# Kernel tuning notes

Measured on AMD Instinct MI355X. Metric: run time of the kernel, lower is better.

The kernel has to match this reference:

```python
import jax, jax.numpy as jnp
import numpy as np

B, QUE, VAL, D = 4, 128, 128, 512

def setup_inputs() -> dict:
    key = jax.random.key(0)
    k = jax.random.split(key, 8)
    return {
        "qs_1": jax.random.normal(k[0], (B, QUE, D), jnp.float32),
        "qs_2": jax.random.normal(k[1], (B, QUE, D), jnp.float32),  # unused by forward, kept for signature fidelity
        "ks":   jax.random.normal(k[2], (B, VAL, D), jnp.float32),
        "vs":   jax.random.normal(k[3], (B, VAL, D), jnp.float32),
        "sg_mask": jax.random.randint(k[4], (B, VAL), 0, 2).astype(bool),  # True = masked
        "W1":  jax.random.normal(k[5], (D, D), jnp.float32) / np.sqrt(D),
        "b1":  jnp.zeros((D,), jnp.float32),
        "Wse": jax.random.normal(k[6], (D, D), jnp.float32) / np.sqrt(D),
        "bse": jnp.zeros((D,), jnp.float32),
        "W2":  jax.random.normal(k[7], (D, 1), jnp.float32) / np.sqrt(D),
        "b2":  jnp.zeros((1,), jnp.float32),
    }

def reference(qs_1, qs_2, ks, vs, sg_mask, W1, b1, Wse, bse, W2, b2):
    # Pairwise query-key elementwise product: [B, que, val, d]
    x = qs_1[:, :, None, :] * ks[:, None, :, :]
    # linear1: Linear(d,d) + ReLU (dropout = identity at eval)
    h = jax.nn.relu(jnp.einsum('bqvd,de->bqve', x, W1) + b1)
    # linear2: Linear(d,1) + ReLU -> scalar score per (q, v) pair
    s = jax.nn.relu(jnp.einsum('bqvd,do->bqvo', h, W2) + b2)[..., 0]  # [B, que, val]
    m = sg_mask[:, None, :]                      # [B, 1, val], True = masked out
    # masked mean of h over the val axis (masked_fill(0) then divide by valid count)
    h = jnp.where(m[..., None], 0.0, h)
    denom = jnp.sum(~sg_mask, axis=-1).astype(h.dtype)      # [B]
    mean = h.sum(axis=2) / denom[:, None, None]             # [B, que, d]
    # squeeze-excitation gate: sigmoid(relu(Linear(d,d)))
    gate = jax.nn.sigmoid(jax.nn.relu(mean @ Wse + bse))    # [B, que, d]
    # masked softmax over val, weighted sum of values
    s = jnp.where(m, -1e9, s)
    w = jax.nn.softmax(s, axis=-1)                          # [B, que, val]
    out = jnp.einsum('bqv,bvd->bqd', w, vs)                 # [B, que, d]
    return gate * out
```

## Files before the change

kernel.cpp:

```cpp
#include <hip/hip_runtime.h>
#include <stdint.h>
#include <stddef.h>

#define BDIM 4
#define QUE  128
#define VAL  128
#define DD   512
#define BQ   (BDIM*QUE)
#define BK   64

typedef float    f32x4 __attribute__((ext_vector_type(4)));
typedef float    f32x2 __attribute__((ext_vector_type(2)));
typedef _Float16 f16x8 __attribute__((ext_vector_type(8)));
typedef _Float16 f16x4 __attribute__((ext_vector_type(4)));
typedef _Float16 f16x2 __attribute__((ext_vector_type(2)));

typedef const __attribute__((address_space(1))) void* gas_ptr;
typedef __attribute__((address_space(3))) void*       las_ptr;

__device__ __forceinline__ void async_copy16(const void* g, void* l) {
    __builtin_amdgcn_global_load_lds((gas_ptr)g, (las_ptr)l, 16, 0, 0);
}

__global__ __launch_bounds__(256) void prep_kernel(const float* __restrict__ W1,
                                                   _Float16* __restrict__ W1T,
                                                   const float* __restrict__ Wse,
                                                   _Float16* __restrict__ WseT,
                                                   const float* __restrict__ vs,
                                                   _Float16* __restrict__ vsT,
                                                   const float* __restrict__ qs1,
                                                   _Float16* __restrict__ qH,
                                                   const float* __restrict__ ks,
                                                   _Float16* __restrict__ ksH) {
    const int gx = blockIdx.x, gy = blockIdx.y;
    if (gy >= 36) {
        const float* src = (gy == 36) ? qs1 : ks;
        _Float16*    dst = (gy == 36) ? qH  : ksH;
        size_t base = (size_t)gx * 16384 + threadIdx.x * 4;
        #pragma unroll 4
        for (int i = 0; i < 16; ++i) {
            f32x4 w = *(const f32x4*)(src + base + (size_t)i * 1024);
            f16x4 h;
            h[0] = (_Float16)w[0]; h[1] = (_Float16)w[1];
            h[2] = (_Float16)w[2]; h[3] = (_Float16)w[3];
            *(f16x4*)(dst + base + (size_t)i * 1024) = h;
        }
        return;
    }
    __shared__ float tile[32][33];
    const int tx = threadIdx.x & 31;
    const int ty = threadIdx.x >> 5;
    if (gy < 32) {
        const float* src = (gy < 16) ? W1  : Wse;
        _Float16*    dst = (gy < 16) ? W1T : WseT;
        int a0 = gx * 32;
        int b0 = (gy & 15) * 32;
        #pragma unroll
        for (int r = 0; r < 4; ++r)
            tile[ty + r*8][tx] = src[(size_t)(a0 + ty + r*8) * DD + b0 + tx];
        __syncthreads();
        #pragma unroll
        for (int r = 0; r < 4; ++r) {
            int el = ty + r*8;
            dst[(size_t)(b0 + el) * DD + a0 + tx] = (_Float16)tile[tx][el];
        }
    } else {
        int bb = gy - 32;
        const float* src = vs  + (size_t)bb * VAL * DD;
        _Float16*    dst = vsT + (size_t)bb * DD * VAL;
        int b0 = gx * 32;
        for (int vt = 0; vt < 4; ++vt) {
            int a0 = vt * 32;
            __syncthreads();
            #pragma unroll
            for (int r = 0; r < 4; ++r)
                tile[ty + r*8][tx] = src[(size_t)(a0 + ty + r*8) * DD + b0 + tx];
            __syncthreads();
            #pragma unroll
            for (int r = 0; r < 4; ++r) {
                int el = ty + r*8;
                dst[(size_t)(b0 + el) * VAL + a0 + tx] = (_Float16)tile[tx][el];
            }
        }
    }
}

__global__ __launch_bounds__(512, 4) void gemm_h_kernel(
    const _Float16* __restrict__ qH,
    const _Float16* __restrict__ ksH,
    const int*   __restrict__ sgmask,
    const _Float16* __restrict__ W1T,
    const float* __restrict__ b1,
    const float* __restrict__ W2,
    float* __restrict__ s_part,
    float* __restrict__ meansum)
{
    __shared__ _Float16 Ah[128 * BK];
    __shared__ _Float16 Bh[256 * BK];
    __shared__ float sred[4][VAL];
    __shared__ float msumLDS[2][256];

    const int tid  = threadIdx.x;
    const int bq   = blockIdx.x;
    const int gy   = blockIdx.y;
    const int b    = bq >> 7;
    const int lane = tid & 63;
    const int wid  = tid >> 6;
    const int wm   = wid >> 2;
    const int wn   = wid & 3;
    const int quad = lane >> 4;
    const int lr   = lane & 15;

    f32x4 acc[4][4];
    #pragma unroll
    for (int i = 0; i < 4; ++i)
        #pragma unroll
        for (int j = 0; j < 4; ++j) acc[i][j] = (f32x4){0.f, 0.f, 0.f, 0.f};

    const int ar0 = tid >> 3;
    const int slt = tid & 7;
    const int ca0 = (slt - (ar0 & 7)) & 7;
    const _Float16* ksrow0 = ksH + ((size_t)b * VAL + ar0)      * DD + ca0 * 8;
    const _Float16* ksrow1 = ksH + ((size_t)b * VAL + 64 + ar0) * DD + ca0 * 8;
    const _Float16* qrow_g = qH  + (size_t)bq * DD + ca0 * 8;
    const int aoff0 = tid * 8;
    const int aoff1 = (512 + tid) * 8;

    const _Float16* gB[4];
    int ldsBoff[4];
    #pragma unroll
    for (int j = 0; j < 4; ++j) {
        int chunk = j * 512 + tid;
        int row   = chunk >> 3;
        int c     = ((chunk & 7) - (row & 7)) & 7;
        gB[j] = W1T + (size_t)(gy * 256 + row) * DD + c * 8;
        ldsBoff[j] = (j * 512 + wid * 64) * 8;
    }

    int faoff[4], fboff[4];
    #pragma unroll
    for (int mt = 0; mt < 4; ++mt) {
        int row = wm * 64 + mt * 16 + lr;
        faoff[mt] = row * BK + (((quad + row) & 7) << 3);
    }
    #pragma unroll
    for (int nt = 0; nt < 4; ++nt) {
        int row = wn * 64 + nt * 16 + lr;
        fboff[nt] = row * BK + (((quad + row) & 7) << 3);
    }

    f16x8 kv0 = *(const f16x8*)(ksrow0);
    f16x8 kv1 = *(const f16x8*)(ksrow1);
    f16x8 qv  = *(const f16x8*)(qrow_g);

    for (int i = 0; i < 8; ++i) {
        const int kk = i * BK;
        #pragma unroll
        for (int j = 0; j < 4; ++j)
            async_copy16(gB[j] + kk, &Bh[ldsBoff[j]]);
        *(f16x8*)&Ah[aoff0] = kv0 * qv;
        *(f16x8*)&Ah[aoff1] = kv1 * qv;
        __syncthreads();

        if (i < 7) {
            kv0 = *(const f16x8*)(ksrow0 + kk + BK);
            kv1 = *(const f16x8*)(ksrow1 + kk + BK);
            qv  = *(const f16x8*)(qrow_g + kk + BK);
        }
        #pragma unroll
        for (int sub = 0; sub < 2; ++sub) {
            const int sx = sub << 5;
            f16x8 fa[4];
            #pragma unroll
            for (int mt = 0; mt < 4; ++mt)
                fa[mt] = *(const f16x8*)&Ah[faoff[mt] ^ sx];
            #pragma unroll
            for (int nt = 0; nt < 4; ++nt) {
                f16x8 fb = *(const f16x8*)&Bh[fboff[nt] ^ sx];
                #pragma unroll
                for (int mt = 0; mt < 4; ++mt)
                    acc[mt][nt] = __builtin_amdgcn_mfma_f32_16x16x32_f16(fa[mt], fb, acc[mt][nt], 0, 0, 0);
            }
        }
        __syncthreads();
    }

    float b1v[4], w2v[4];
    #pragma unroll
    for (int nt = 0; nt < 4; ++nt) {
        int col = gy*256 + wn*64 + nt*16 + lr;
        b1v[nt] = b1[col];
        w2v[nt] = W2[col];
    }
    float msum[4] = {0.f, 0.f, 0.f, 0.f};
    #pragma unroll
    for (int mt = 0; mt < 4; ++mt) {
        #pragma unroll
        for (int reg = 0; reg < 4; ++reg) {
            int v = wm*64 + mt*16 + quad*4 + reg;
            int masked = sgmask[b * VAL + v];
            float sacc = 0.f;
            #pragma unroll
            for (int nt = 0; nt < 4; ++nt) {
                float h = acc[mt][nt][reg] + b1v[nt];
                h = fmaxf(h, 0.f);
                sacc += h * w2v[nt];
                if (!masked) msum[nt] += h;
            }
            sacc += __shfl_xor(sacc, 1);
            sacc += __shfl_xor(sacc, 2);
            sacc += __shfl_xor(sacc, 4);
            sacc += __shfl_xor(sacc, 8);
            if (lr == 0) sred[wn][v] = sacc;
        }
    }
    #pragma unroll
    for (int nt = 0; nt < 4; ++nt) {
        float m = msum[nt];
        m += __shfl_xor(m, 16);
        m += __shfl_xor(m, 32);
        if (lane < 16) msumLDS[wm][wn*64 + nt*16 + lr] = m;
    }
    __syncthreads();
    if (tid < 128) {
        s_part[((size_t)bq * 2 + gy) * VAL + tid] =
            sred[0][tid] + sred[1][tid] + sred[2][tid] + sred[3][tid];
    } else if (tid >= 256) {
        int c = tid - 256;
        meansum[(size_t)bq * DD + gy*256 + c] = msumLDS[0][c] + msumLDS[1][c];
    }
}

#define MPAD 514
#define WPAD 130
__global__ __launch_bounds__(256) void final_kernel(
    const float* __restrict__ s_part,
    const float* __restrict__ msum,
    const int*   __restrict__ sgmask,
    const _Float16* __restrict__ WseT,
    const _Float16* __restrict__ vsT,
    const float* __restrict__ bse,
    const float* __restrict__ b2,
    float* __restrict__ out)
{
    __shared__ _Float16 meanLDS[32 * MPAD];
    __shared__ _Float16 wLDS[32 * WPAD];
    __shared__ _Float16 BLDS[32 * WPAD];

    const int tid  = threadIdx.x;
    const int q0   = blockIdx.x * 32;
    const int d0   = blockIdx.y * 32;
    const int b    = q0 >> 7;
    const int lane = tid & 63;
    const int wid  = tid >> 6;
    const int wm   = wid >> 1, wn = wid & 1;
    const int quad = lane >> 4;
    const int lr   = lane & 15;
    const int r    = tid >> 3;
    const int sl   = tid & 7;

    const float b2v = b2[0];
    const int   bq  = q0 + r;
    const float* sp = s_part + (size_t)bq * 2 * VAL;
    float vals[16];
    int   msk[16];
    float smax = -3.4e38f;
    #pragma unroll
    for (int i4 = 0; i4 < 4; ++i4) {
        f32x4 s0 = *(const f32x4*)(sp + sl*16 + i4*4);
        f32x4 s1 = *(const f32x4*)(sp + VAL + sl*16 + i4*4);
        #pragma unroll
        for (int j = 0; j < 4; ++j) {
            int idx = i4*4 + j;
            int v   = sl*16 + idx;
            float s = fmaxf(s0[j] + s1[j] + b2v, 0.f);
            int m   = sgmask[b * VAL + v];
            msk[idx] = m;
            if (m) s = -1e9f;
            vals[idx] = s;
            smax = fmaxf(smax, s);
        }
    }
    smax = fmaxf(smax, __shfl_xor(smax, 1));
    smax = fmaxf(smax, __shfl_xor(smax, 2));
    smax = fmaxf(smax, __shfl_xor(smax, 4));
    float sume = 0.f, cnt = 0.f;
    #pragma unroll
    for (int i = 0; i < 16; ++i) {
        vals[i] = __expf(vals[i] - smax);
        sume += vals[i];
        cnt  += msk[i] ? 0.f : 1.f;
    }
    sume += __shfl_xor(sume, 1);  cnt += __shfl_xor(cnt, 1);
    sume += __shfl_xor(sume, 2);  cnt += __shfl_xor(cnt, 2);
    sume += __shfl_xor(sume, 4);  cnt += __shfl_xor(cnt, 4);
    const float invse = 1.f / sume;
    const float invd  = 1.f / cnt;
    f16x8 wv0, wv1;
    #pragma unroll
    for (int i = 0; i < 8; ++i) {
        wv0[i] = (_Float16)(vals[i]     * invse);
        wv1[i] = (_Float16)(vals[i + 8] * invse);
    }
    *(f16x8*)&wLDS[r * WPAD + sl*16]     = wv0;
    *(f16x8*)&wLDS[r * WPAD + sl*16 + 8] = wv1;
    const float* mrow = msum + (size_t)bq * DD;
    #pragma unroll
    for (int i = 0; i < 8; ++i) {
        int e = i*64 + sl*8;
        f32x4 m0 = *(const f32x4*)(mrow + e);
        f32x4 m1 = *(const f32x4*)(mrow + e + 4);
        f16x8 mh;
        #pragma unroll
        for (int c = 0; c < 4; ++c) {
            mh[c]     = (_Float16)(m0[c] * invd);
            mh[c + 4] = (_Float16)(m1[c] * invd);
        }
        *(f16x8*)&meanLDS[r * MPAD + e] = mh;
    }
    __syncthreads();

    f32x4 accg = (f32x4){0.f, 0.f, 0.f, 0.f};
    const int a_off = (wm*16 + lr) * MPAD + quad*8;
    const int b_off = (wn*16 + lr) * WPAD + quad*8;
    const int st_off = r * WPAD + sl*16;
    #pragma unroll
    for (int cc = 0; cc < 4; ++cc) {
        const _Float16* wrow = WseT + (size_t)(d0 + r) * DD + cc*128 + sl*16;
        f16x8 bw0 = *(const f16x8*)(wrow);
        f16x8 bw1 = *(const f16x8*)(wrow + 8);
        *(f16x8*)&BLDS[st_off]     = bw0;
        *(f16x8*)&BLDS[st_off + 8] = bw1;
        __syncthreads();
        #pragma unroll
        for (int ks = 0; ks < 4; ++ks) {
            f16x8 fa = *(const f16x8*)&meanLDS[a_off + cc*128 + ks*32];
            f16x8 fb = *(const f16x8*)&BLDS[b_off + ks*32];
            accg = __builtin_amdgcn_mfma_f32_16x16x32_f16(fa, fb, accg, 0, 0, 0);
        }
        __syncthreads();
    }

    {
        const _Float16* vrow = vsT + ((size_t)b * DD + d0 + r) * VAL + sl*16;
        f16x8 bv0 = *(const f16x8*)(vrow);
        f16x8 bv1 = *(const f16x8*)(vrow + 8);
        *(f16x8*)&BLDS[st_off]     = bv0;
        *(f16x8*)&BLDS[st_off + 8] = bv1;
    }
    __syncthreads();
    f32x4 acco = (f32x4){0.f, 0.f, 0.f, 0.f};
    const int w_off = (wm*16 + lr) * WPAD + quad*8;
    #pragma unroll
    for (int ks = 0; ks < 4; ++ks) {
        f16x8 fa = *(const f16x8*)&wLDS[w_off + ks*32];
        f16x8 fb = *(const f16x8*)&BLDS[b_off + ks*32];
        acco = __builtin_amdgcn_mfma_f32_16x16x32_f16(fa, fb, acco, 0, 0, 0);
    }

    const int d = d0 + wn*16 + lr;
    const float bsev = bse[d];
    #pragma unroll
    for (int reg = 0; reg < 4; ++reg) {
        int q = q0 + wm*16 + quad*4 + reg;
        float g = fmaxf(accg[reg] + bsev, 0.f);
        g = 1.f / (1.f + __expf(-g));
        out[(size_t)q * DD + d] = g * acco[reg];
    }
}

extern "C" void kernel_launch(void* const* d_in, const int* in_sizes, int n_in,
                              void* d_out, int out_size, void* d_ws, size_t ws_size,
                              hipStream_t stream) {
    (void)in_sizes; (void)n_in; (void)out_size; (void)ws_size;
    const float* qs1 = (const float*)d_in[0];
    const float* ks  = (const float*)d_in[2];
    const float* vs  = (const float*)d_in[3];
    const int*   sg  = (const int*)d_in[4];
    const float* W1  = (const float*)d_in[5];
    const float* b1  = (const float*)d_in[6];
    const float* Wse = (const float*)d_in[7];
    const float* bse = (const float*)d_in[8];
    const float* W2  = (const float*)d_in[9];
    const float* b2  = (const float*)d_in[10];
    float* out = (float*)d_out;

    char* ws = (char*)d_ws;
    _Float16* W1T    = (_Float16*)(ws);
    _Float16* WseT   = (_Float16*)(ws + (512 << 10));
    _Float16* vsT    = (_Float16*)(ws + (1 << 20));
    float*    s_part = (float*)(ws + (1536 << 10));
    float*    msum   = (float*)(ws + (2 << 20));
    _Float16* qH     = (_Float16*)(ws + (3 << 20));
    _Float16* ksH    = (_Float16*)(ws + (3 << 20) + (512 << 10));

    prep_kernel<<<dim3(16, 38), 256, 0, stream>>>(W1, W1T, Wse, WseT, vs, vsT,
                                                  qs1, qH, ks, ksH);
    gemm_h_kernel<<<dim3(BQ, 2), 512, 0, stream>>>(qH, ksH, sg, W1T, b1, W2, s_part, msum);
    final_kernel<<<dim3(16, 16), 256, 0, stream>>>(s_part, msum, sg, WseT, vsT, bse, b2, out);
}
```

Measured before the change: 128.4 us.

## Split prep work across more blocks and preload final-kernel operands into LDS

```diff
diff --git a/kernel.cpp b/kernel.cpp
--- a/kernel.cpp
+++ b/kernel.cpp
@@ -10,10 +10,8 @@
 #define BK   64
 
 typedef float    f32x4 __attribute__((ext_vector_type(4)));
-typedef float    f32x2 __attribute__((ext_vector_type(2)));
 typedef _Float16 f16x8 __attribute__((ext_vector_type(8)));
 typedef _Float16 f16x4 __attribute__((ext_vector_type(4)));
-typedef _Float16 f16x2 __attribute__((ext_vector_type(2)));
 
 typedef const __attribute__((address_space(1))) void* gas_ptr;
 typedef __attribute__((address_space(3))) void*       las_ptr;
@@ -33,12 +31,12 @@
                                                    const float* __restrict__ ks,
                                                    _Float16* __restrict__ ksH) {
     const int gx = blockIdx.x, gy = blockIdx.y;
-    if (gy >= 36) {
-        const float* src = (gy == 36) ? qs1 : ks;
-        _Float16*    dst = (gy == 36) ? qH  : ksH;
-        size_t base = (size_t)gx * 16384 + threadIdx.x * 4;
-        #pragma unroll 4
-        for (int i = 0; i < 16; ++i) {
+    if (gy >= 48) {
+        const float* src = (gy < 50) ? qs1 : ks;
+        _Float16*    dst = (gy < 50) ? qH  : ksH;
+        size_t base = ((size_t)(gy & 1) * 16 + gx) * 8192 + threadIdx.x * 4;
+        #pragma unroll
+        for (int i = 0; i < 8; ++i) {
             f32x4 w = *(const f32x4*)(src + base + (size_t)i * 1024);
             f16x4 h;
             h[0] = (_Float16)w[0]; h[1] = (_Float16)w[1];
@@ -50,38 +48,33 @@
     __shared__ float tile[32][33];
     const int tx = threadIdx.x & 31;
     const int ty = threadIdx.x >> 5;
+    const float* src;
+    _Float16*    dst;
+    int a0, b0, dstride;
     if (gy < 32) {
-        const float* src = (gy < 16) ? W1  : Wse;
-        _Float16*    dst = (gy < 16) ? W1T : WseT;
-        int a0 = gx * 32;
-        int b0 = (gy & 15) * 32;
-        #pragma unroll
-        for (int r = 0; r < 4; ++r)
-            tile[ty + r*8][tx] = src[(size_t)(a0 + ty + r*8) * DD + b0 + tx];
-        __syncthreads();
-        #pragma unroll
-        for (int r = 0; r < 4; ++r) {
-            int el = ty + r*8;
-            dst[(size_t)(b0 + el) * DD + a0 + tx] = (_Float16)tile[tx][el];
-        }
+        src = (gy < 16) ? W1  : Wse;
+        dst = (gy < 16) ? W1T : WseT;
+        a0 = gx * 32;
+        b0 = (gy & 15) * 32;
+        dstride = DD;
     } else {
-        int bb = gy - 32;
-        const float* src = vs  + (size_t)bb * VAL * DD;
-        _Float16*    dst = vsT + (size_t)bb * DD * VAL;
-        int b0 = gx * 32;
-        for (int vt = 0; vt < 4; ++vt) {
-            int a0 = vt * 32;
-            __syncthreads();
-            #pragma unroll
-            for (int r = 0; r < 4; ++r)
-                tile[ty + r*8][tx] = src[(size_t)(a0 + ty + r*8) * DD + b0 + tx];
-            __syncthreads();
-            #pragma unroll
-            for (int r = 0; r < 4; ++r) {
-                int el = ty + r*8;
-                dst[(size_t)(b0 + el) * VAL + a0 + tx] = (_Float16)tile[tx][el];
-            }
-        }
+        const int j  = gy - 32;
+        const int bb = j >> 2;
+        const int vt = j & 3;
+        src = vs  + (size_t)bb * VAL * DD;
+        dst = vsT + (size_t)bb * DD * VAL;
+        a0 = vt * 32;
+        b0 = gx * 32;
+        dstride = VAL;
+    }
+    #pragma unroll
+    for (int r = 0; r < 4; ++r)
+        tile[ty + r*8][tx] = src[(size_t)(a0 + ty + r*8) * DD + b0 + tx];
+    __syncthreads();
+    #pragma unroll
+    for (int r = 0; r < 4; ++r) {
+        int el = ty + r*8;
+        dst[(size_t)(b0 + el) * dstride + a0 + tx] = (_Float16)tile[tx][el];
     }
 }
 
@@ -244,8 +237,9 @@
     float* __restrict__ out)
 {
     __shared__ _Float16 meanLDS[32 * MPAD];
+    __shared__ _Float16 BW[32 * MPAD];
     __shared__ _Float16 wLDS[32 * WPAD];
-    __shared__ _Float16 BLDS[32 * WPAD];
+    __shared__ _Float16 BV[32 * WPAD];
 
     const int tid  = threadIdx.x;
     const int q0   = blockIdx.x * 32;
@@ -259,6 +253,22 @@
     const int r    = tid >> 3;
     const int sl   = tid & 7;
 
+    {
+        const _Float16* wrow = WseT + (size_t)(d0 + r) * DD + sl*16;
+        #pragma unroll
+        for (int cc = 0; cc < 4; ++cc) {
+            f16x8 bw0 = *(const f16x8*)(wrow + cc*128);
+            f16x8 bw1 = *(const f16x8*)(wrow + cc*128 + 8);
+            *(f16x8*)&BW[r * MPAD + cc*128 + sl*16]     = bw0;
+            *(f16x8*)&BW[r * MPAD + cc*128 + sl*16 + 8] = bw1;
+        }
+        const _Float16* vrow = vsT + ((size_t)b * DD + d0 + r) * VAL + sl*16;
+        f16x8 bv0 = *(const f16x8*)(vrow);
+        f16x8 bv1 = *(const f16x8*)(vrow + 8);
+        *(f16x8*)&BV[r * WPAD + sl*16]     = bv0;
+        *(f16x8*)&BV[r * WPAD + sl*16 + 8] = bv1;
+    }
+
     const float b2v = b2[0];
     const int   bq  = q0 + r;
     const float* sp = s_part + (size_t)bq * 2 * VAL;
@@ -318,43 +328,33 @@
         }
         *(f16x8*)&meanLDS[r * MPAD + e] = mh;
     }
+
     __syncthreads();
 
-    f32x4 accg = (f32x4){0.f, 0.f, 0.f, 0.f};
+    f32x4 accg0 = (f32x4){0.f, 0.f, 0.f, 0.f};
+    f32x4 accg1 = (f32x4){0.f, 0.f, 0.f, 0.f};
     const int a_off = (wm*16 + lr) * MPAD + quad*8;
-    const int b_off = (wn*16 + lr) * WPAD + quad*8;
-    const int st_off = r * WPAD + sl*16;
+    const int bg_off = (wn*16 + lr) * MPAD + quad*8;
     #pragma unroll
     for (int cc = 0; cc < 4; ++cc) {
-        const _Float16* wrow = WseT + (size_t)(d0 + r) * DD + cc*128 + sl*16;
-        f16x8 bw0 = *(const f16x8*)(wrow);
-        f16x8 bw1 = *(const f16x8*)(wrow + 8);
-        *(f16x8*)&BLDS[st_off]     = bw0;
-        *(f16x8*)&BLDS[st_off + 8] = bw1;
-        __syncthreads();
         #pragma unroll
         for (int ks = 0; ks < 4; ++ks) {
             f16x8 fa = *(const f16x8*)&meanLDS[a_off + cc*128 + ks*32];
-            f16x8 fb = *(const f16x8*)&BLDS[b_off + ks*32];
-            accg = __builtin_amdgcn_mfma_f32_16x16x32_f16(fa, fb, accg, 0, 0, 0);
-        }
-        __syncthreads();
-    }
-
-    {
-        const _Float16* vrow = vsT + ((size_t)b * DD + d0 + r) * VAL + sl*16;
-        f16x8 bv0 = *(const f16x8*)(vrow);
-        f16x8 bv1 = *(const f16x8*)(vrow + 8);
-        *(f16x8*)&BLDS[st_off]     = bv0;
-        *(f16x8*)&BLDS[st_off + 8] = bv1;
-    }
-    __syncthreads();
+            f16x8 fb = *(const f16x8*)&BW[bg_off + cc*128 + ks*32];
+            if (((cc*4 + ks) & 1) == 0)
+                accg0 = __builtin_amdgcn_mfma_f32_16x16x32_f16(fa, fb, accg0, 0, 0, 0);
+            else
+                accg1 = __builtin_amdgcn_mfma_f32_16x16x32_f16(fa, fb, accg1, 0, 0, 0);
+        }
+    }
+
     f32x4 acco = (f32x4){0.f, 0.f, 0.f, 0.f};
     const int w_off = (wm*16 + lr) * WPAD + quad*8;
+    const int bv_off = (wn*16 + lr) * WPAD + quad*8;
     #pragma unroll
     for (int ks = 0; ks < 4; ++ks) {
         f16x8 fa = *(const f16x8*)&wLDS[w_off + ks*32];
-        f16x8 fb = *(const f16x8*)&BLDS[b_off + ks*32];
+        f16x8 fb = *(const f16x8*)&BV[bv_off + ks*32];
         acco = __builtin_amdgcn_mfma_f32_16x16x32_f16(fa, fb, acco, 0, 0, 0);
     }
 
@@ -363,7 +363,7 @@
     #pragma unroll
     for (int reg = 0; reg < 4; ++reg) {
         int q = q0 + wm*16 + quad*4 + reg;
-        float g = fmaxf(accg[reg] + bsev, 0.f);
+        float g = fmaxf(accg0[reg] + accg1[reg] + bsev, 0.f);
         g = 1.f / (1.f + __expf(-g));
         out[(size_t)q * DD + d] = g * acco[reg];
     }
@@ -394,7 +394,7 @@
     _Float16* qH     = (_Float16*)(ws + (3 << 20));
     _Float16* ksH    = (_Float16*)(ws + (3 << 20) + (512 << 10));
 
-    prep_kernel<<<dim3(16, 38), 256, 0, stream>>>(W1, W1T, Wse, WseT, vs, vsT,
+    prep_kernel<<<dim3(16, 52), 256, 0, stream>>>(W1, W1T, Wse, WseT, vs, vsT,
                                                   qs1, qH, ks, ksH);
     gemm_h_kernel<<<dim3(BQ, 2), 512, 0, stream>>>(qH, ksH, sg, W1T, b1, W2, s_part, msum);
     final_kernel<<<dim3(16, 16), 256, 0, stream>>>(s_part, msum, sg, WseT, vsT, bse, b2, out);
```

Result: no change. 126.0 us (-1.8%).

## Fuse final gating and softmax-weighted sum into the H GEMM kernel

Applied to the files above, without the earlier changes.

```diff
diff --git a/kernel.cpp b/kernel.cpp
--- a/kernel.cpp
+++ b/kernel.cpp
@@ -10,7 +10,6 @@
 #define BK   64
 
 typedef float    f32x4 __attribute__((ext_vector_type(4)));
-typedef float    f32x2 __attribute__((ext_vector_type(2)));
 typedef _Float16 f16x8 __attribute__((ext_vector_type(8)));
 typedef _Float16 f16x4 __attribute__((ext_vector_type(4)));
 typedef _Float16 f16x2 __attribute__((ext_vector_type(2)));
@@ -26,19 +25,18 @@
                                                    _Float16* __restrict__ W1T,
                                                    const float* __restrict__ Wse,
                                                    _Float16* __restrict__ WseT,
-                                                   const float* __restrict__ vs,
-                                                   _Float16* __restrict__ vsT,
                                                    const float* __restrict__ qs1,
                                                    _Float16* __restrict__ qH,
                                                    const float* __restrict__ ks,
                                                    _Float16* __restrict__ ksH) {
     const int gx = blockIdx.x, gy = blockIdx.y;
-    if (gy >= 36) {
-        const float* src = (gy == 36) ? qs1 : ks;
-        _Float16*    dst = (gy == 36) ? qH  : ksH;
-        size_t base = (size_t)gx * 16384 + threadIdx.x * 4;
-        #pragma unroll 4
-        for (int i = 0; i < 16; ++i) {
+    if (gy >= 32) {
+        const int jj = gy - 32;
+        const float* src = (jj < 2) ? qs1 : ks;
+        _Float16*    dst = (jj < 2) ? qH  : ksH;
+        size_t base = ((size_t)(jj & 1) * 16 + gx) * 8192 + threadIdx.x * 4;
+        #pragma unroll
+        for (int i = 0; i < 8; ++i) {
             f32x4 w = *(const f32x4*)(src + base + (size_t)i * 1024);
             f16x4 h;
             h[0] = (_Float16)w[0]; h[1] = (_Float16)w[1];
@@ -50,38 +48,18 @@
     __shared__ float tile[32][33];
     const int tx = threadIdx.x & 31;
     const int ty = threadIdx.x >> 5;
-    if (gy < 32) {
-        const float* src = (gy < 16) ? W1  : Wse;
-        _Float16*    dst = (gy < 16) ? W1T : WseT;
-        int a0 = gx * 32;
-        int b0 = (gy & 15) * 32;
-        #pragma unroll
-        for (int r = 0; r < 4; ++r)
-            tile[ty + r*8][tx] = src[(size_t)(a0 + ty + r*8) * DD + b0 + tx];
-        __syncthreads();
-        #pragma unroll
-        for (int r = 0; r < 4; ++r) {
-            int el = ty + r*8;
-            dst[(size_t)(b0 + el) * DD + a0 + tx] = (_Float16)tile[tx][el];
-        }
-    } else {
-        int bb = gy - 32;
-        const float* src = vs  + (size_t)bb * VAL * DD;
-        _Float16*    dst = vsT + (size_t)bb * DD * VAL;
-        int b0 = gx * 32;
-        for (int vt = 0; vt < 4; ++vt) {
-            int a0 = vt * 32;
-            __syncthreads();
-            #pragma unroll
-            for (int r = 0; r < 4; ++r)
-                tile[ty + r*8][tx] = src[(size_t)(a0 + ty + r*8) * DD + b0 + tx];
-            __syncthreads();
-            #pragma unroll
-            for (int r = 0; r < 4; ++r) {
-                int el = ty + r*8;
-                dst[(size_t)(b0 + el) * VAL + a0 + tx] = (_Float16)tile[tx][el];
-            }
-        }
+    const float* src = (gy < 16) ? W1  : Wse;
+    _Float16*    dst = (gy < 16) ? W1T : WseT;
+    const int a0 = gx * 32;
+    const int b0 = (gy & 15) * 32;
+    #pragma unroll
+    for (int r = 0; r < 4; ++r)
+        tile[ty + r*8][tx] = src[(size_t)(a0 + ty + r*8) * DD + b0 + tx];
+    __syncthreads();
+    #pragma unroll
+    for (int r = 0; r < 4; ++r) {
+        int el = ty + r*8;
+        dst[(size_t)(b0 + el) * DD + a0 + tx] = (_Float16)tile[tx][el];
     }
 }
 
@@ -92,17 +70,22 @@
     const _Float16* __restrict__ W1T,
     const float* __restrict__ b1,
     const float* __restrict__ W2,
-    float* __restrict__ s_part,
-    float* __restrict__ meansum)
+    const _Float16* __restrict__ WseT,
+    const float* __restrict__ bse,
+    const float* __restrict__ b2,
+    const float* __restrict__ vs,
+    float* __restrict__ out)
 {
     __shared__ _Float16 Ah[128 * BK];
     __shared__ _Float16 Bh[256 * BK];
-    __shared__ float sred[4][VAL];
-    __shared__ float msumLDS[2][256];
+    __shared__ float sredP[4][VAL];
+    __shared__ float msumP2[2][DD];
+    __shared__ float w_lds[VAL];
+    __shared__ _Float16 mean_h[DD];
+    __shared__ float scal[1];
 
     const int tid  = threadIdx.x;
     const int bq   = blockIdx.x;
-    const int gy   = blockIdx.y;
     const int b    = bq >> 7;
     const int lane = tid & 63;
     const int wid  = tid >> 6;
@@ -110,12 +93,6 @@
     const int wn   = wid & 3;
     const int quad = lane >> 4;
     const int lr   = lane & 15;
-
-    f32x4 acc[4][4];
-    #pragma unroll
-    for (int i = 0; i < 4; ++i)
-        #pragma unroll
-        for (int j = 0; j < 4; ++j) acc[i][j] = (f32x4){0.f, 0.f, 0.f, 0.f};
 
     const int ar0 = tid >> 3;
     const int slt = tid & 7;
@@ -133,7 +110,7 @@
         int chunk = j * 512 + tid;
         int row   = chunk >> 3;
         int c     = ((chunk & 7) - (row & 7)) & 7;
-        gB[j] = W1T + (size_t)(gy * 256 + row) * DD + c * 8;
+        gB[j] = W1T + (size_t)row * DD + c * 8;
         ldsBoff[j] = (j * 512 + wid * 64) * 8;
     }
 
@@ -149,224 +126,156 @@
         fboff[nt] = row * BK + (((quad + row) & 7) << 3);
     }
 
-    f16x8 kv0 = *(const f16x8*)(ksrow0);
-    f16x8 kv1 = *(const f16x8*)(ksrow1);
-    f16x8 qv  = *(const f16x8*)(qrow_g);
-
-    for (int i = 0; i < 8; ++i) {
-        const int kk = i * BK;
-        #pragma unroll
-        for (int j = 0; j < 4; ++j)
-            async_copy16(gB[j] + kk, &Bh[ldsBoff[j]]);
-        *(f16x8*)&Ah[aoff0] = kv0 * qv;
-        *(f16x8*)&Ah[aoff1] = kv1 * qv;
-        __syncthreads();
-
-        if (i < 7) {
-            kv0 = *(const f16x8*)(ksrow0 + kk + BK);
-            kv1 = *(const f16x8*)(ksrow1 + kk + BK);
-            qv  = *(const f16x8*)(qrow_g + kk + BK);
-        }
-        #pragma unroll
-        for (int sub = 0; sub < 2; ++sub) {
-            const int sx = sub << 5;
-            f16x8 fa[4];
-            #pragma unroll
-            for (int mt = 0; mt < 4; ++mt)
-                fa[mt] = *(const f16x8*)&Ah[faoff[mt] ^ sx];
-            #pragma unroll
-            for (int nt = 0; nt < 4; ++nt) {
-                f16x8 fb = *(const f16x8*)&Bh[fboff[nt] ^ sx];
+    for (int pass = 0; pass < 2; ++pass) {
+        const size_t poff = (size_t)pass * 256 * DD;
+
+        f32x4 acc[4][4];
+        #pragma unroll
+        for (int i = 0; i < 4; ++i)
+            #pragma unroll
+            for (int j = 0; j < 4; ++j) acc[i][j] = (f32x4){0.f, 0.f, 0.f, 0.f};
+
+        f16x8 kv0 = *(const f16x8*)(ksrow0);
+        f16x8 kv1 = *(const f16x8*)(ksrow1);
+        f16x8 qv  = *(const f16x8*)(qrow_g);
+
+        for (int i = 0; i < 8; ++i) {
+            const int kk = i * BK;
+            #pragma unroll
+            for (int j = 0; j < 4; ++j)
+                async_copy16(gB[j] + poff + kk, &Bh[ldsBoff[j]]);
+            *(f16x8*)&Ah[aoff0] = kv0 * qv;
+            *(f16x8*)&Ah[aoff1] = kv1 * qv;
+            __syncthreads();
+
+            if (i < 7) {
+                kv0 = *(const f16x8*)(ksrow0 + kk + BK);
+                kv1 = *(const f16x8*)(ksrow1 + kk + BK);
+                qv  = *(const f16x8*)(qrow_g + kk + BK);
+            }
+            #pragma unroll
+            for (int sub = 0; sub < 2; ++sub) {
+                const int sx = sub << 5;
+                f16x8 fa[4];
                 #pragma unroll
                 for (int mt = 0; mt < 4; ++mt)
-                    acc[mt][nt] = __builtin_amdgcn_mfma_f32_16x16x32_f16(fa[mt], fb, acc[mt][nt], 0, 0, 0);
+                    fa[mt] = *(const f16x8*)&Ah[faoff[mt] ^ sx];
+                #pragma unroll
+                for (int nt = 0; nt < 4; ++nt) {
+                    f16x8 fb = *(const f16x8*)&Bh[fboff[nt] ^ sx];
+                    #pragma unroll
+                    for (int mt = 0; mt < 4; ++mt)
+                        acc[mt][nt] = __builtin_amdgcn_mfma_f32_16x16x32_f16(fa[mt], fb, acc[mt][nt], 0, 0, 0);
+                }
             }
-        }
-        __syncthreads();
-    }
-
-    float b1v[4], w2v[4];
-    #pragma unroll
-    for (int nt = 0; nt < 4; ++nt) {
-        int col = gy*256 + wn*64 + nt*16 + lr;
-        b1v[nt] = b1[col];
-        w2v[nt] = W2[col];
-    }
-    float msum[4] = {0.f, 0.f, 0.f, 0.f};
-    #pragma unroll
-    for (int mt = 0; mt < 4; ++mt) {
-        #pragma unroll
-        for (int reg = 0; reg < 4; ++reg) {
-            int v = wm*64 + mt*16 + quad*4 + reg;
-            int masked = sgmask[b * VAL + v];
-            float sacc = 0.f;
-            #pragma unroll
-            for (int nt = 0; nt < 4; ++nt) {
-                float h = acc[mt][nt][reg] + b1v[nt];
-                h = fmaxf(h, 0.f);
-                sacc += h * w2v[nt];
-                if (!masked) msum[nt] += h;
+            __syncthreads();
+        }
+
+        float b1v[4], w2v[4];
+        #pragma unroll
+        for (int nt = 0; nt < 4; ++nt) {
+            int col = pass*256 + wn*64 + nt*16 + lr;
+            b1v[nt] = b1[col];
+            w2v[nt] = W2[col];
+        }
+        float msm[4] = {0.f, 0.f, 0.f, 0.f};
+        #pragma unroll
+        for (int mt = 0; mt < 4; ++mt) {
+            #pragma unroll
+            for (int reg = 0; reg < 4; ++reg) {
+                int v = wm*64 + mt*16 + quad*4 + reg;
+                int masked = sgmask[b * VAL + v];
+                float sacc = 0.f;
+                #pragma unroll
+                for (int nt = 0; nt < 4; ++nt) {
+                    float h = acc[mt][nt][reg] + b1v[nt];
+                    h = fmaxf(h, 0.f);
+                    sacc += h * w2v[nt];
+                    if (!masked) msm[nt] += h;
+                }
+                sacc += __shfl_xor(sacc, 1);
+                sacc += __shfl_xor(sacc, 2);
+                sacc += __shfl_xor(sacc, 4);
+                sacc += __shfl_xor(sacc, 8);
+                if (lr == 0) {
+                    if (pass == 0) sredP[wn][v]  = sacc;
+                    else           sredP[wn][v] += sacc;
+                }
             }
-            sacc += __shfl_xor(sacc, 1);
-            sacc += __shfl_xor(sacc, 2);
-            sacc += __shfl_xor(sacc, 4);
-            sacc += __shfl_xor(sacc, 8);
-            if (lr == 0) sred[wn][v] = sacc;
-        }
-    }
-    #pragma unroll
-    for (int nt = 0; nt < 4; ++nt) {
-        float m = msum[nt];
-        m += __shfl_xor(m, 16);
-        m += __shfl_xor(m, 32);
-        if (lane < 16) msumLDS[wm][wn*64 + nt*16 + lr] = m;
-    }
+        }
+        #pragma unroll
+        for (int nt = 0; nt < 4; ++nt) {
+            float m = msm[nt];
+            m += __shfl_xor(m, 16);
+            m += __shfl_xor(m, 32);
+            if (lane < 16) msumP2[wm][pass*256 + wn*64 + nt*16 + lr] = m;
+        }
+    }
+
     __syncthreads();
-    if (tid < 128) {
-        s_part[((size_t)bq * 2 + gy) * VAL + tid] =
-            sred[0][tid] + sred[1][tid] + sred[2][tid] + sred[3][tid];
-    } else if (tid >= 256) {
-        int c = tid - 256;
-        meansum[(size_t)bq * DD + gy*256 + c] = msumLDS[0][c] + msumLDS[1][c];
-    }
-}
-
-#define MPAD 514
-#define WPAD 130
-__global__ __launch_bounds__(256) void final_kernel(
-    const float* __restrict__ s_part,
-    const float* __restrict__ msum,
-    const int*   __restrict__ sgmask,
-    const _Float16* __restrict__ WseT,
-    const _Float16* __restrict__ vsT,
-    const float* __restrict__ bse,
-    const float* __restrict__ b2,
-    float* __restrict__ out)
-{
-    __shared__ _Float16 meanLDS[32 * MPAD];
-    __shared__ _Float16 wLDS[32 * WPAD];
-    __shared__ _Float16 BLDS[32 * WPAD];
-
-    const int tid  = threadIdx.x;
-    const int q0   = blockIdx.x * 32;
-    const int d0   = blockIdx.y * 32;
-    const int b    = q0 >> 7;
-    const int lane = tid & 63;
-    const int wid  = tid >> 6;
-    const int wm   = wid >> 1, wn = wid & 1;
-    const int quad = lane >> 4;
-    const int lr   = lane & 15;
-    const int r    = tid >> 3;
-    const int sl   = tid & 7;
 
     const float b2v = b2[0];
-    const int   bq  = q0 + r;
-    const float* sp = s_part + (size_t)bq * 2 * VAL;
-    float vals[16];
-    int   msk[16];
-    float smax = -3.4e38f;
-    #pragma unroll
-    for (int i4 = 0; i4 < 4; ++i4) {
-        f32x4 s0 = *(const f32x4*)(sp + sl*16 + i4*4);
-        f32x4 s1 = *(const f32x4*)(sp + VAL + sl*16 + i4*4);
-        #pragma unroll
-        for (int j = 0; j < 4; ++j) {
-            int idx = i4*4 + j;
-            int v   = sl*16 + idx;
-            float s = fmaxf(s0[j] + s1[j] + b2v, 0.f);
-            int m   = sgmask[b * VAL + v];
-            msk[idx] = m;
-            if (m) s = -1e9f;
-            vals[idx] = s;
-            smax = fmaxf(smax, s);
-        }
-    }
-    smax = fmaxf(smax, __shfl_xor(smax, 1));
-    smax = fmaxf(smax, __shfl_xor(smax, 2));
-    smax = fmaxf(smax, __shfl_xor(smax, 4));
-    float sume = 0.f, cnt = 0.f;
-    #pragma unroll
-    for (int i = 0; i < 16; ++i) {
-        vals[i] = __expf(vals[i] - smax);
-        sume += vals[i];
-        cnt  += msk[i] ? 0.f : 1.f;
-    }
-    sume += __shfl_xor(sume, 1);  cnt += __shfl_xor(cnt, 1);
-    sume += __shfl_xor(sume, 2);  cnt += __shfl_xor(cnt, 2);
-    sume += __shfl_xor(sume, 4);  cnt += __shfl_xor(cnt, 4);
-    const float invse = 1.f / sume;
-    const float invd  = 1.f / cnt;
-    f16x8 wv0, wv1;
-    #pragma unroll
-    for (int i = 0; i < 8; ++i) {
-        wv0[i] = (_Float16)(vals[i]     * invse);
-        wv1[i] = (_Float16)(vals[i + 8] * invse);
-    }
-    *(f16x8*)&wLDS[r * WPAD + sl*16]     = wv0;
-    *(f16x8*)&wLDS[r * WPAD + sl*16 + 8] = wv1;
-    const float* mrow = msum + (size_t)bq * DD;
-    #pragma unroll
-    for (int i = 0; i < 8; ++i) {
-        int e = i*64 + sl*8;
-        f32x4 m0 = *(const f32x4*)(mrow + e);
-        f32x4 m1 = *(const f32x4*)(mrow + e + 4);
-        f16x8 mh;
-        #pragma unroll
-        for (int c = 0; c < 4; ++c) {
-            mh[c]     = (_Float16)(m0[c] * invd);
-            mh[c + 4] = (_Float16)(m1[c] * invd);
-        }
-        *(f16x8*)&meanLDS[r * MPAD + e] = mh;
+    if (wid == 0) {
+        const int v0 = lane, v1 = lane + 64;
+        float s0 = sredP[0][v0] + sredP[1][v0] + sredP[2][v0] + sredP[3][v0] + b2v;
+        float s1 = sredP[0][v1] + sredP[1][v1] + sredP[2][v1] + sredP[3][v1] + b2v;
+        s0 = fmaxf(s0, 0.f);  s1 = fmaxf(s1, 0.f);
+        const int m0 = sgmask[b * VAL + v0], m1 = sgmask[b * VAL + v1];
+        if (m0) s0 = -1e9f;
+        if (m1) s1 = -1e9f;
+        float mx = fmaxf(s0, s1);
+        #pragma unroll
+        for (int off = 1; off < 64; off <<= 1)
+            mx = fmaxf(mx, __shfl_xor(mx, off));
+        float e0 = __expf(s0 - mx), e1 = __expf(s1 - mx);
+        float sm = e0 + e1;
+        float cn = (m0 ? 0.f : 1.f) + (m1 ? 0.f : 1.f);
+        #pragma unroll
+        for (int off = 1; off < 64; off <<= 1) {
+            sm += __shfl_xor(sm, off);
+            cn += __shfl_xor(cn, off);
+        }
+        const float inv = 1.f / sm;
+        w_lds[v0] = e0 * inv;
+        w_lds[v1] = e1 * inv;
+        if (lane == 0) scal[0] = 1.f / cn;
     }
     __syncthreads();
 
-    f32x4 accg = (f32x4){0.f, 0.f, 0.f, 0.f};
-    const int a_off = (wm*16 + lr) * MPAD + quad*8;
-    const int b_off = (wn*16 + lr) * WPAD + quad*8;
-    const int st_off = r * WPAD + sl*16;
-    #pragma unroll
-    for (int cc = 0; cc < 4; ++cc) {
-        const _Float16* wrow = WseT + (size_t)(d0 + r) * DD + cc*128 + sl*16;
-        f16x8 bw0 = *(const f16x8*)(wrow);
-        f16x8 bw1 = *(const f16x8*)(wrow + 8);
-        *(f16x8*)&BLDS[st_off]     = bw0;
-        *(f16x8*)&BLDS[st_off + 8] = bw1;
-        __syncthreads();
-        #pragma unroll
-        for (int ks = 0; ks < 4; ++ks) {
-            f16x8 fa = *(const f16x8*)&meanLDS[a_off + cc*128 + ks*32];
-            f16x8 fb = *(const f16x8*)&BLDS[b_off + ks*32];
-            accg = __builtin_amdgcn_mfma_f32_16x16x32_f16(fa, fb, accg, 0, 0, 0);
-        }
-        __syncthreads();
-    }
-
+    const float invd = scal[0];
+    mean_h[tid] = (_Float16)((msumP2[0][tid] + msumP2[1][tid]) * invd);
+    __syncthreads();
+
+    float ga = 0.f;
     {
-        const _Float16* vrow = vsT + ((size_t)b * DD + d0 + r) * VAL + sl*16;
-        f16x8 bv0 = *(const f16x8*)(vrow);
-        f16x8 bv1 = *(const f16x8*)(vrow + 8);
-        *(f16x8*)&BLDS[st_off]     = bv0;
-        *(f16x8*)&BLDS[st_off + 8] = bv1;
-    }
-    __syncthreads();
-    f32x4 acco = (f32x4){0.f, 0.f, 0.f, 0.f};
-    const int w_off = (wm*16 + lr) * WPAD + quad*8;
-    #pragma unroll
-    for (int ks = 0; ks < 4; ++ks) {
-        f16x8 fa = *(const f16x8*)&wLDS[w_off + ks*32];
-        f16x8 fb = *(const f16x8*)&BLDS[b_off + ks*32];
-        acco = __builtin_amdgcn_mfma_f32_16x16x32_f16(fa, fb, acco, 0, 0, 0);
-    }
-
-    const int d = d0 + wn*16 + lr;
-    const float bsev = bse[d];
-    #pragma unroll
-    for (int reg = 0; reg < 4; ++reg) {
-        int q = q0 + wm*16 + quad*4 + reg;
-        float g = fmaxf(accg[reg] + bsev, 0.f);
-        g = 1.f / (1.f + __expf(-g));
-        out[(size_t)q * DD + d] = g * acco[reg];
-    }
+        const _Float16* wrow = WseT + (size_t)tid * DD;
+        #pragma unroll 4
+        for (int e = 0; e < DD; e += 8) {
+            f16x8 me = *(const f16x8*)&mean_h[e];
+            f16x8 we = *(const f16x8*)(wrow + e);
+            #pragma unroll
+            for (int p2 = 0; p2 < 4; ++p2) {
+                f16x2 ma = {me[2*p2], me[2*p2+1]};
+                f16x2 wa = {we[2*p2], we[2*p2+1]};
+#if __has_builtin(__builtin_amdgcn_fdot2)
+                ga = __builtin_amdgcn_fdot2(ma, wa, ga, false);
+#else
+                ga += (float)ma[0] * (float)wa[0] + (float)ma[1] * (float)wa[1];
+#endif
+            }
+        }
+    }
+    float gate = fmaxf(ga + bse[tid], 0.f);
+    gate = 1.f / (1.f + __expf(-gate));
+
+    float oa = 0.f;
+    {
+        const float* vsb = vs + (size_t)b * VAL * DD + tid;
+        #pragma unroll 8
+        for (int v = 0; v < VAL; ++v)
+            oa += w_lds[v] * vsb[(size_t)v * DD];
+    }
+    out[(size_t)bq * DD + tid] = gate * oa;
 }
 
 extern "C" void kernel_launch(void* const* d_in, const int* in_sizes, int n_in,
@@ -388,14 +297,11 @@
     char* ws = (char*)d_ws;
     _Float16* W1T    = (_Float16*)(ws);
     _Float16* WseT   = (_Float16*)(ws + (512 << 10));
-    _Float16* vsT    = (_Float16*)(ws + (1 << 20));
-    float*    s_part = (float*)(ws + (1536 << 10));
-    float*    msum   = (float*)(ws + (2 << 20));
-    _Float16* qH     = (_Float16*)(ws + (3 << 20));
-    _Float16* ksH    = (_Float16*)(ws + (3 << 20) + (512 << 10));
-
-    prep_kernel<<<dim3(16, 38), 256, 0, stream>>>(W1, W1T, Wse, WseT, vs, vsT,
+    _Float16* qH     = (_Float16*)(ws + (1 << 20));
+    _Float16* ksH    = (_Float16*)(ws + (1536 << 10));
+
+    prep_kernel<<<dim3(16, 36), 256, 0, stream>>>(W1, W1T, Wse, WseT,
                                                   qs1, qH, ks, ksH);
-    gemm_h_kernel<<<dim3(BQ, 2), 512, 0, stream>>>(qH, ksH, sg, W1T, b1, W2, s_part, msum);
-    final_kernel<<<dim3(16, 16), 256, 0, stream>>>(s_part, msum, sg, WseT, vsT, bse, b2, out);
+    gemm_h_kernel<<<dim3(BQ), 512, 0, stream>>>(qH, ksH, sg, W1T, b1, W2,
+                                                WseT, bse, b2, vs, out);
 }
```

Measured after the change: 174.4 us. 1.36x slower.
